# Kernel tuning notes

Measured on AMD Instinct MI355X. Metric: run time of the kernel, lower is better.

## Reference

```python
import jax, jax.numpy as jnp
import numpy as np

T = 2097152  # conversation length (even, per assert in the original forward)


def setup_inputs() -> dict:
    key = jax.random.key(0)
    k0, k1, k2, k3, k4, k5 = jax.random.split(key, 6)
    emission_scores = jax.random.normal(k0, (T, 2), dtype=jnp.float32)
    label = jax.random.randint(k1, (T,), 0, 2)
    who2who_state = jax.random.randint(k2, (T,), 0, 2)
    position_state = jax.random.randint(k3, (T,), 0, 19)
    # first step must use the zero (padding) transition matrix, per the original assert
    who2who_state = who2who_state.at[0].set(2)
    position_state = position_state.at[0].set(19)
    # learned params: matrice_u2s, matrice_s2u stacked; 19 position matrices stacked
    who2who_params = jax.random.normal(k4, (2, 2, 2), dtype=jnp.float32)
    position_params = jax.random.normal(k5, (19, 2, 2), dtype=jnp.float32)
    return dict(emission_scores=emission_scores, label=label,
                who2who_state=who2who_state, position_state=position_state,
                who2who_params=who2who_params, position_params=position_params)


def reference(emission_scores, label, who2who_state, position_state,
              who2who_params, position_params):
    dt = emission_scores.dtype
    pad = jnp.zeros((1, 2, 2), dtype=dt)
    who2who_sub = jnp.concatenate([who2who_params, pad], axis=0)    # [3,2,2]
    position_sub = jnp.concatenate([position_params, pad], axis=0)  # [20,2,2]
    # per-step combined transition matrices (Who2who_PositionCRF): [T,2,2]
    trans = who2who_sub[who2who_state] + position_sub[position_state]

    Tlen = emission_scores.shape[0]
    idx = jnp.arange(Tlen)
    sum_emission = jnp.sum(emission_scores[idx, label])
    # transitions are used for index > 0 with (label[t-1], label[t])
    sum_transition = jnp.sum(trans[1:][jnp.arange(Tlen - 1), label[:-1], label[1:]])
    gold_score = sum_emission + sum_transition

    # CRF forward (partition) recursion: alpha'[j] = logsumexp_i(alpha[i] + em[t,j] + trans[t,i,j])
    def step(alpha, xt):
        em_t, tr_t = xt  # [2], [2,2]
        new_alpha = jax.nn.logsumexp(alpha[:, None] + em_t[None, :] + tr_t, axis=0)
        return new_alpha, None

    alpha0 = jnp.zeros((2,), dtype=dt)
    alpha, _ = jax.lax.scan(step, alpha0, (emission_scores, trans))
    total_score = jax.nn.logsumexp(alpha)

    return jnp.stack([gold_score, total_score])
```

## Files before the change

kernel.cpp:

```cpp
#include <hip/hip_runtime.h>

#define T_LEN   2097152
#define CHUNK   8
#define BLOCK   256
#define NBLK    (T_LEN / (CHUNK * BLOCK))
#define NWAVE   (BLOCK / 64)
#define FINAL_PER (NBLK / 256)

#define LOG2E 1.44269504088896340736f
#define LN2   0.69314718055994530942f

__device__ __forceinline__ float fexp2(float x) {
#if __has_builtin(__builtin_amdgcn_exp2f)
    return __builtin_amdgcn_exp2f(x);
#else
    return __expf(x * LN2);
#endif
}
__device__ __forceinline__ float flog2(float x) {
#if __has_builtin(__builtin_amdgcn_logf)
    return __builtin_amdgcn_logf(x);
#else
    return __logf(x) * LOG2E;
#endif
}

__device__ __forceinline__ float lse2b(float x, float y) {
    float m = fmaxf(x, y);
    float d = fminf(x, y) - m;
    return m + flog2(1.0f + fexp2(d));
}

struct M2 { float a, b, c, d; };

__device__ __forceinline__ M2 mm(const M2 A, const M2 B) {
    M2 C;
    C.a = lse2b(A.a + B.a, A.b + B.c);
    C.b = lse2b(A.a + B.b, A.b + B.d);
    C.c = lse2b(A.c + B.a, A.d + B.c);
    C.d = lse2b(A.c + B.b, A.d + B.d);
    return C;
}

__device__ __forceinline__ void wave_reduce(M2& P, float& g, int lane) {
    #pragma unroll
    for (int m = 1; m < 64; m <<= 1) {
        M2 O;
        O.a = __shfl_xor(P.a, m);
        O.b = __shfl_xor(P.b, m);
        O.c = __shfl_xor(P.c, m);
        O.d = __shfl_xor(P.d, m);
        g  += __shfl_xor(g, m);
        bool hi = (lane & m) != 0;
        M2 X, Y;
        X.a = hi ? O.a : P.a;  X.b = hi ? O.b : P.b;
        X.c = hi ? O.c : P.c;  X.d = hi ? O.d : P.d;
        Y.a = hi ? P.a : O.a;  Y.b = hi ? P.b : O.b;
        Y.c = hi ? P.c : O.c;  Y.d = hi ? P.d : O.d;
        P = mm(X, Y);
    }
}

__global__ __launch_bounds__(BLOCK) void crf_partial(
    const float* __restrict__ em,
    const int*   __restrict__ label,
    const int*   __restrict__ wst,
    const int*   __restrict__ pst,
    const float* __restrict__ w2w,
    const float* __restrict__ pos,
    float* __restrict__ outP,
    float* __restrict__ outG)
{
    __shared__ float4 comb[60];
    __shared__ float4 wPs[NWAVE];
    __shared__ float  wGs[NWAVE];

    const int tid = threadIdx.x;
    if (tid < 60) {
        const int w = tid / 20, p = tid % 20;
        float v0 = 0.f, v1 = 0.f, v2 = 0.f, v3 = 0.f;
        if (w < 2)  { v0 += w2w[w*4+0]; v1 += w2w[w*4+1]; v2 += w2w[w*4+2]; v3 += w2w[w*4+3]; }
        if (p < 19) { v0 += pos[p*4+0]; v1 += pos[p*4+1]; v2 += pos[p*4+2]; v3 += pos[p*4+3]; }
        comb[tid] = make_float4(v0 * LOG2E, v1 * LOG2E, v2 * LOG2E, v3 * LOG2E);
    }
    __syncthreads();

    const int t0 = (blockIdx.x * BLOCK + tid) * CHUNK;

    const float4* emv = (const float4*)(em + 2 * (size_t)t0);
    float4 E0 = emv[0], E1 = emv[1], E2 = emv[2], E3 = emv[3];
    const int4* lv = (const int4*)(label + t0);
    const int4* wv = (const int4*)(wst   + t0);
    const int4* pv = (const int4*)(pst   + t0);
    int4 L0 = lv[0], L1 = lv[1];
    int4 W0 = wv[0], W1 = wv[1];
    int4 Pq0 = pv[0], Pq1 = pv[1];
    int prev = (t0 == 0) ? 0 : label[t0 - 1];

    E0.x *= LOG2E; E0.y *= LOG2E; E0.z *= LOG2E; E0.w *= LOG2E;
    E1.x *= LOG2E; E1.y *= LOG2E; E1.z *= LOG2E; E1.w *= LOG2E;
    E2.x *= LOG2E; E2.y *= LOG2E; E2.z *= LOG2E; E2.w *= LOG2E;
    E3.x *= LOG2E; E3.y *= LOG2E; E3.z *= LOG2E; E3.w *= LOG2E;

    float4 c0 = comb[W0.x*20 + Pq0.x];
    float4 c1 = comb[W0.y*20 + Pq0.y];
    float4 c2 = comb[W0.z*20 + Pq0.z];
    float4 c3 = comb[W0.w*20 + Pq0.w];
    float4 c4 = comb[W1.x*20 + Pq1.x];
    float4 c5 = comb[W1.y*20 + Pq1.y];
    float4 c6 = comb[W1.z*20 + Pq1.z];
    float4 c7 = comb[W1.w*20 + Pq1.w];

    float Pa, Pb, Pc, Pd, g;

    Pa = E0.x + c0.x;  Pb = E0.y + c0.y;
    Pc = E0.x + c0.z;  Pd = E0.y + c0.w;
    {
        const int l = L0.x;
        g  = l ? E0.y : E0.x;
        g += prev ? (l ? c0.w : c0.z) : (l ? c0.y : c0.x);
        prev = l;
    }

#define STEP(e0v, e1v, cc, ll)                                             \
    {                                                                      \
        const float e0 = (e0v), e1 = (e1v);                                \
        const float4 c = (cc);                                             \
        const int l = (ll);                                                \
        g += l ? e1 : e0;                                                  \
        g += prev ? (l ? c.w : c.z) : (l ? c.y : c.x);                     \
        prev = l;                                                          \
        float na = e0 + lse2b(Pa + c.x, Pb + c.z);                         \
        float nb = e1 + lse2b(Pa + c.y, Pb + c.w);                         \
        float nc = e0 + lse2b(Pc + c.x, Pd + c.z);                         \
        float nd = e1 + lse2b(Pc + c.y, Pd + c.w);                         \
        Pa = na; Pb = nb; Pc = nc; Pd = nd;                                \
    }

    STEP(E0.z, E0.w, c1, L0.y)
    STEP(E1.x, E1.y, c2, L0.z)
    STEP(E1.z, E1.w, c3, L0.w)
    STEP(E2.x, E2.y, c4, L1.x)
    STEP(E2.z, E2.w, c5, L1.y)
    STEP(E3.x, E3.y, c6, L1.z)
    STEP(E3.z, E3.w, c7, L1.w)
#undef STEP

    M2 P = { Pa, Pb, Pc, Pd };
    const int lane = tid & 63;
    wave_reduce(P, g, lane);

    const int wid = tid >> 6;
    if (lane == 0) { wPs[wid] = make_float4(P.a, P.b, P.c, P.d); wGs[wid] = g; }
    __syncthreads();
    if (tid == 0) {
        float4 q = wPs[0];
        M2 R = { q.x, q.y, q.z, q.w };
        float gg = wGs[0];
        #pragma unroll
        for (int w = 1; w < NWAVE; ++w) {
            float4 t = wPs[w];
            M2 B = { t.x, t.y, t.z, t.w };
            R = mm(R, B);
            gg += wGs[w];
        }
        ((float4*)outP)[blockIdx.x] = make_float4(R.a, R.b, R.c, R.d);
        outG[blockIdx.x] = gg;
    }
}

__global__ __launch_bounds__(256) void crf_final(
    const float* __restrict__ inP,
    const float* __restrict__ inG,
    float* __restrict__ out)
{
    __shared__ float4 wPs[4];
    __shared__ float  wGs[4];

    const int tid  = threadIdx.x;
    const int base = tid * FINAL_PER;

    float4 q = ((const float4*)inP)[base];
    M2 P = { q.x, q.y, q.z, q.w };
    float g = inG[base];
    #pragma unroll
    for (int k = 1; k < FINAL_PER; ++k) {
        float4 r = ((const float4*)inP)[base + k];
        M2 B = { r.x, r.y, r.z, r.w };
        P = mm(P, B);
        g += inG[base + k];
    }

    const int lane = tid & 63;
    wave_reduce(P, g, lane);

    const int wid = tid >> 6;
    if (lane == 0) { wPs[wid] = make_float4(P.a, P.b, P.c, P.d); wGs[wid] = g; }
    __syncthreads();
    if (tid == 0) {
        float4 q0 = wPs[0];
        M2 R = { q0.x, q0.y, q0.z, q0.w };
        float gg = wGs[0];
        #pragma unroll
        for (int w = 1; w < 4; ++w) {
            float4 t = wPs[w];
            M2 B = { t.x, t.y, t.z, t.w };
            R = mm(R, B);
            gg += wGs[w];
        }
        out[0] = gg * LN2;
        out[1] = lse2b(lse2b(R.a, R.b), lse2b(R.c, R.d)) * LN2;
    }
}

extern "C" void kernel_launch(void* const* d_in, const int* in_sizes, int n_in,
                              void* d_out, int out_size, void* d_ws, size_t ws_size,
                              hipStream_t stream) {
    const float* em    = (const float*)d_in[0];
    const int*   label = (const int*)  d_in[1];
    const int*   wst   = (const int*)  d_in[2];
    const int*   pst   = (const int*)  d_in[3];
    const float* w2w   = (const float*)d_in[4];
    const float* pos   = (const float*)d_in[5];
    float* out = (float*)d_out;

    float* outP = (float*)d_ws;
    float* outG = outP + NBLK * 4;

    crf_partial<<<NBLK, BLOCK, 0, stream>>>(em, label, wst, pst, w2w, pos, outP, outG);
    crf_final<<<1, 256, 0, stream>>>(outP, outG, out);
}
```

Measured before the change: 18.59 us.

## Switch CRF scan to linear-domain products with exponent renorm and fuse final reduction

The log-semiring 2x2 matrix products, which need an exp2/log2 pair per element, are replaced by ordinary linear-domain products. Emissions and transitions are exponentiated once, and overflow is managed by periodically pulling out power-of-two exponents into an integer. The chunk per thread is doubled to 16. The separate final kernel is replaced by a last-block-done atomic counter in the same kernel, which adds a memset launch. This cuts transcendental work and a kernel launch, at the cost of precision risk from linear-domain accumulation between renorms.

Result: slower. 29.94 us (+61.0%).

```diff
diff --git a/kernel.cpp b/kernel.cpp
--- a/kernel.cpp
+++ b/kernel.cpp
@@ -1,67 +1,60 @@
 #include <hip/hip_runtime.h>
 
 #define T_LEN   2097152
-#define CHUNK   8
+#define CHUNK   16
 #define BLOCK   256
 #define NBLK    (T_LEN / (CHUNK * BLOCK))
 #define NWAVE   (BLOCK / 64)
-#define FINAL_PER (NBLK / 256)
 
 #define LOG2E 1.44269504088896340736f
 #define LN2   0.69314718055994530942f
 
-__device__ __forceinline__ float fexp2(float x) {
 #if __has_builtin(__builtin_amdgcn_exp2f)
-    return __builtin_amdgcn_exp2f(x);
+__device__ __forceinline__ float fexp2(float x) { return __builtin_amdgcn_exp2f(x); }
 #else
-    return __expf(x * LN2);
+__device__ __forceinline__ float fexp2(float x) { return exp2f(x); }
 #endif
-}
-__device__ __forceinline__ float flog2(float x) {
 #if __has_builtin(__builtin_amdgcn_logf)
-    return __builtin_amdgcn_logf(x);
+__device__ __forceinline__ float flog2(float x) { return __builtin_amdgcn_logf(x); }
 #else
-    return __logf(x) * LOG2E;
+__device__ __forceinline__ float flog2(float x) { return log2f(x); }
 #endif
-}
-
-__device__ __forceinline__ float lse2b(float x, float y) {
-    float m = fmaxf(x, y);
-    float d = fminf(x, y) - m;
-    return m + flog2(1.0f + fexp2(d));
-}
-
-struct M2 { float a, b, c, d; };
-
-__device__ __forceinline__ M2 mm(const M2 A, const M2 B) {
-    M2 C;
-    C.a = lse2b(A.a + B.a, A.b + B.c);
-    C.b = lse2b(A.a + B.b, A.b + B.d);
-    C.c = lse2b(A.c + B.a, A.d + B.c);
-    C.d = lse2b(A.c + B.b, A.d + B.d);
-    return C;
-}
-
-__device__ __forceinline__ void wave_reduce(M2& P, float& g, int lane) {
+
+__device__ __forceinline__ void renorm4(float& a, float& b, float& c, float& d, int& e2) {
+    float mx = fmaxf(fmaxf(a, b), fmaxf(c, d));
+    int ex = (__float_as_int(mx) >> 23) & 0xff;
+    float s = __int_as_float((254 - ex) << 23);
+    a *= s; b *= s; c *= s; d *= s;
+    e2 += ex - 127;
+}
+__device__ __forceinline__ void renorm1(float& a, int& e2) {
+    int ex = (__float_as_int(a) >> 23) & 0xff;
+    float s = __int_as_float((254 - ex) << 23);
+    a *= s;
+    e2 += ex - 127;
+}
+
+__device__ __forceinline__ void wave_reduce_lin(float& Pa, float& Pb, float& Pc, float& Pd,
+                                                int& e2, float& g, int lane) {
     #pragma unroll
     for (int m = 1; m < 64; m <<= 1) {
-        M2 O;
-        O.a = __shfl_xor(P.a, m);
-        O.b = __shfl_xor(P.b, m);
-        O.c = __shfl_xor(P.c, m);
-        O.d = __shfl_xor(P.d, m);
-        g  += __shfl_xor(g, m);
-        bool hi = (lane & m) != 0;
-        M2 X, Y;
-        X.a = hi ? O.a : P.a;  X.b = hi ? O.b : P.b;
-        X.c = hi ? O.c : P.c;  X.d = hi ? O.d : P.d;
-        Y.a = hi ? P.a : O.a;  Y.b = hi ? P.b : O.b;
-        Y.c = hi ? P.c : O.c;  Y.d = hi ? P.d : O.d;
-        P = mm(X, Y);
-    }
-}
-
-__global__ __launch_bounds__(BLOCK) void crf_partial(
+        float Oa = __shfl_xor(Pa, m), Ob = __shfl_xor(Pb, m);
+        float Oc = __shfl_xor(Pc, m), Od = __shfl_xor(Pd, m);
+        int   Oe = __shfl_xor(e2, m);
+        g += __shfl_xor(g, m);
+        const bool hi = (lane & m) != 0;
+        float Xa = hi?Oa:Pa, Xb = hi?Ob:Pb, Xc = hi?Oc:Pc, Xd = hi?Od:Pd;
+        float Ya = hi?Pa:Oa, Yb = hi?Pb:Ob, Yc = hi?Pc:Oc, Yd = hi?Pd:Od;
+        Pa = Xa*Ya + Xb*Yc;
+        Pb = Xa*Yb + Xb*Yd;
+        Pc = Xc*Ya + Xd*Yc;
+        Pd = Xc*Yb + Xd*Yd;
+        e2 += Oe;
+        renorm4(Pa, Pb, Pc, Pd, e2);
+    }
+}
+
+__global__ __launch_bounds__(BLOCK) void crf_fused(
     const float* __restrict__ em,
     const int*   __restrict__ label,
     const int*   __restrict__ wst,
@@ -69,11 +62,16 @@
     const float* __restrict__ w2w,
     const float* __restrict__ pos,
     float* __restrict__ outP,
-    float* __restrict__ outG)
+    int*   __restrict__ outE,
+    float* __restrict__ outG,
+    unsigned* __restrict__ cnt,
+    float* __restrict__ out)
 {
-    __shared__ float4 comb[60];
+    __shared__ float4 combExp[60];
     __shared__ float4 wPs[NWAVE];
+    __shared__ int    wEs[NWAVE];
     __shared__ float  wGs[NWAVE];
+    __shared__ int    shLast;
 
     const int tid = threadIdx.x;
     if (tid < 60) {
@@ -81,7 +79,8 @@
         float v0 = 0.f, v1 = 0.f, v2 = 0.f, v3 = 0.f;
         if (w < 2)  { v0 += w2w[w*4+0]; v1 += w2w[w*4+1]; v2 += w2w[w*4+2]; v3 += w2w[w*4+3]; }
         if (p < 19) { v0 += pos[p*4+0]; v1 += pos[p*4+1]; v2 += pos[p*4+2]; v3 += pos[p*4+3]; }
-        comb[tid] = make_float4(v0 * LOG2E, v1 * LOG2E, v2 * LOG2E, v3 * LOG2E);
+        combExp[tid] = make_float4(fexp2(v0 * LOG2E), fexp2(v1 * LOG2E),
+                                   fexp2(v2 * LOG2E), fexp2(v3 * LOG2E));
     }
     __syncthreads();
 
@@ -89,128 +88,138 @@
 
     const float4* emv = (const float4*)(em + 2 * (size_t)t0);
     float4 E0 = emv[0], E1 = emv[1], E2 = emv[2], E3 = emv[3];
+    float4 E4 = emv[4], E5 = emv[5], E6 = emv[6], E7 = emv[7];
     const int4* lv = (const int4*)(label + t0);
     const int4* wv = (const int4*)(wst   + t0);
     const int4* pv = (const int4*)(pst   + t0);
-    int4 L0 = lv[0], L1 = lv[1];
-    int4 W0 = wv[0], W1 = wv[1];
-    int4 Pq0 = pv[0], Pq1 = pv[1];
+    int4 L0 = lv[0], L1 = lv[1], L2 = lv[2], L3 = lv[3];
+    int4 W0 = wv[0], W1 = wv[1], W2 = wv[2], W3 = wv[3];
+    int4 Q0 = pv[0], Q1 = pv[1], Q2 = pv[2], Q3 = pv[3];
     int prev = (t0 == 0) ? 0 : label[t0 - 1];
 
-    E0.x *= LOG2E; E0.y *= LOG2E; E0.z *= LOG2E; E0.w *= LOG2E;
-    E1.x *= LOG2E; E1.y *= LOG2E; E1.z *= LOG2E; E1.w *= LOG2E;
-    E2.x *= LOG2E; E2.y *= LOG2E; E2.z *= LOG2E; E2.w *= LOG2E;
-    E3.x *= LOG2E; E3.y *= LOG2E; E3.z *= LOG2E; E3.w *= LOG2E;
-
-    float4 c0 = comb[W0.x*20 + Pq0.x];
-    float4 c1 = comb[W0.y*20 + Pq0.y];
-    float4 c2 = comb[W0.z*20 + Pq0.z];
-    float4 c3 = comb[W0.w*20 + Pq0.w];
-    float4 c4 = comb[W1.x*20 + Pq1.x];
-    float4 c5 = comb[W1.y*20 + Pq1.y];
-    float4 c6 = comb[W1.z*20 + Pq1.z];
-    float4 c7 = comb[W1.w*20 + Pq1.w];
-
-    float Pa, Pb, Pc, Pd, g;
-
-    Pa = E0.x + c0.x;  Pb = E0.y + c0.y;
-    Pc = E0.x + c0.z;  Pd = E0.y + c0.w;
-    {
-        const int l = L0.x;
-        g  = l ? E0.y : E0.x;
-        g += prev ? (l ? c0.w : c0.z) : (l ? c0.y : c0.x);
-        prev = l;
-    }
-
-#define STEP(e0v, e1v, cc, ll)                                             \
+    float Pa = 1.f, Pb = 0.f, Pc = 0.f, Pd = 1.f;
+    int   e2 = 0;
+    float gEm  = 0.f;
+    float gLin = 1.f;
+    int   eg   = 0;
+
+#define STEP(e0v, e1v, wI, pI, lI)                                         \
     {                                                                      \
         const float e0 = (e0v), e1 = (e1v);                                \
-        const float4 c = (cc);                                             \
-        const int l = (ll);                                                \
-        g += l ? e1 : e0;                                                  \
-        g += prev ? (l ? c.w : c.z) : (l ? c.y : c.x);                     \
+        const float f0 = fexp2(e0 * LOG2E);                                \
+        const float f1 = fexp2(e1 * LOG2E);                                \
+        const float4 X = combExp[(wI)*20 + (pI)];                          \
+        const int l = (lI);                                                \
+        gEm += l ? e1 : e0;                                                \
+        gLin *= prev ? (l ? X.w : X.z) : (l ? X.y : X.x);                  \
         prev = l;                                                          \
-        float na = e0 + lse2b(Pa + c.x, Pb + c.z);                         \
-        float nb = e1 + lse2b(Pa + c.y, Pb + c.w);                         \
-        float nc = e0 + lse2b(Pc + c.x, Pd + c.z);                         \
-        float nd = e1 + lse2b(Pc + c.y, Pd + c.w);                         \
+        float na = (Pa*X.x + Pb*X.z) * f0;                                 \
+        float nb = (Pa*X.y + Pb*X.w) * f1;                                 \
+        float nc = (Pc*X.x + Pd*X.z) * f0;                                 \
+        float nd = (Pc*X.y + Pd*X.w) * f1;                                 \
         Pa = na; Pb = nb; Pc = nc; Pd = nd;                                \
     }
-
-    STEP(E0.z, E0.w, c1, L0.y)
-    STEP(E1.x, E1.y, c2, L0.z)
-    STEP(E1.z, E1.w, c3, L0.w)
-    STEP(E2.x, E2.y, c4, L1.x)
-    STEP(E2.z, E2.w, c5, L1.y)
-    STEP(E3.x, E3.y, c6, L1.z)
-    STEP(E3.z, E3.w, c7, L1.w)
+#define GROUP(Ea, Eb, L, W, Q)                                             \
+    STEP(Ea.x, Ea.y, W.x, Q.x, L.x)                                        \
+    STEP(Ea.z, Ea.w, W.y, Q.y, L.y)                                        \
+    STEP(Eb.x, Eb.y, W.z, Q.z, L.z)                                        \
+    STEP(Eb.z, Eb.w, W.w, Q.w, L.w)                                        \
+    renorm4(Pa, Pb, Pc, Pd, e2);                                           \
+    renorm1(gLin, eg);
+
+    GROUP(E0, E1, L0, W0, Q0)
+    GROUP(E2, E3, L1, W1, Q1)
+    GROUP(E4, E5, L2, W2, Q2)
+    GROUP(E6, E7, L3, W3, Q3)
+#undef GROUP
 #undef STEP
 
-    M2 P = { Pa, Pb, Pc, Pd };
+    float g = gEm + ((float)eg + flog2(gLin)) * LN2;
+
     const int lane = tid & 63;
-    wave_reduce(P, g, lane);
+    wave_reduce_lin(Pa, Pb, Pc, Pd, e2, g, lane);
 
     const int wid = tid >> 6;
-    if (lane == 0) { wPs[wid] = make_float4(P.a, P.b, P.c, P.d); wGs[wid] = g; }
+    if (lane == 0) { wPs[wid] = make_float4(Pa, Pb, Pc, Pd); wEs[wid] = e2; wGs[wid] = g; }
     __syncthreads();
     if (tid == 0) {
         float4 q = wPs[0];
-        M2 R = { q.x, q.y, q.z, q.w };
-        float gg = wGs[0];
+        float Ra = q.x, Rb = q.y, Rc = q.z, Rd = q.w;
+        int   re = wEs[0];
+        float rg = wGs[0];
         #pragma unroll
         for (int w = 1; w < NWAVE; ++w) {
             float4 t = wPs[w];
-            M2 B = { t.x, t.y, t.z, t.w };
-            R = mm(R, B);
-            gg += wGs[w];
+            float Ba = t.x, Bb = t.y, Bc = t.z, Bd = t.w;
+            float Ca = Ra*Ba + Rb*Bc;
+            float Cb = Ra*Bb + Rb*Bd;
+            float Cc = Rc*Ba + Rd*Bc;
+            float Cd = Rc*Bb + Rd*Bd;
+            Ra = Ca; Rb = Cb; Rc = Cc; Rd = Cd;
+            re += wEs[w];
+            renorm4(Ra, Rb, Rc, Rd, re);
+            rg += wGs[w];
         }
-        ((float4*)outP)[blockIdx.x] = make_float4(R.a, R.b, R.c, R.d);
-        outG[blockIdx.x] = gg;
-    }
-}
-
-__global__ __launch_bounds__(256) void crf_final(
-    const float* __restrict__ inP,
-    const float* __restrict__ inG,
-    float* __restrict__ out)
-{
-    __shared__ float4 wPs[4];
-    __shared__ float  wGs[4];
-
-    const int tid  = threadIdx.x;
-    const int base = tid * FINAL_PER;
-
-    float4 q = ((const float4*)inP)[base];
-    M2 P = { q.x, q.y, q.z, q.w };
-    float g = inG[base];
-    #pragma unroll
-    for (int k = 1; k < FINAL_PER; ++k) {
-        float4 r = ((const float4*)inP)[base + k];
-        M2 B = { r.x, r.y, r.z, r.w };
-        P = mm(P, B);
-        g += inG[base + k];
-    }
-
-    const int lane = tid & 63;
-    wave_reduce(P, g, lane);
-
-    const int wid = tid >> 6;
-    if (lane == 0) { wPs[wid] = make_float4(P.a, P.b, P.c, P.d); wGs[wid] = g; }
+        ((float4*)outP)[blockIdx.x] = make_float4(Ra, Rb, Rc, Rd);
+        outE[blockIdx.x] = re;
+        outG[blockIdx.x] = rg;
+    }
+
+    if (tid == 0) {
+        __threadfence();
+        unsigned old = atomicAdd(cnt, 1u);
+        shLast = (old == NBLK - 1) ? 1 : 0;
+    }
     __syncthreads();
-    if (tid == 0) {
-        float4 q0 = wPs[0];
-        M2 R = { q0.x, q0.y, q0.z, q0.w };
-        float gg = wGs[0];
-        #pragma unroll
-        for (int w = 1; w < 4; ++w) {
-            float4 t = wPs[w];
-            M2 B = { t.x, t.y, t.z, t.w };
-            R = mm(R, B);
-            gg += wGs[w];
+    if (!shLast) return;
+    __threadfence();
+
+#define ALDF(p) __hip_atomic_load((p), __ATOMIC_RELAXED, __HIP_MEMORY_SCOPE_AGENT)
+    {
+        const int i0 = 2 * tid, i1 = i0 + 1;
+        float Aa = ALDF(outP + 4*i0 + 0), Ab = ALDF(outP + 4*i0 + 1);
+        float Ac = ALDF(outP + 4*i0 + 2), Ad = ALDF(outP + 4*i0 + 3);
+        float Ba = ALDF(outP + 4*i1 + 0), Bb = ALDF(outP + 4*i1 + 1);
+        float Bc = ALDF(outP + 4*i1 + 2), Bd = ALDF(outP + 4*i1 + 3);
+        int   ea = ALDF(outE + i0), eb = ALDF(outE + i1);
+        float ga = ALDF(outG + i0), gb = ALDF(outG + i1);
+
+        float Pa2 = Aa*Ba + Ab*Bc;
+        float Pb2 = Aa*Bb + Ab*Bd;
+        float Pc2 = Ac*Ba + Ad*Bc;
+        float Pd2 = Ac*Bb + Ad*Bd;
+        int   e2f = ea + eb;
+        renorm4(Pa2, Pb2, Pc2, Pd2, e2f);
+        float gf = ga + gb;
+
+        wave_reduce_lin(Pa2, Pb2, Pc2, Pd2, e2f, gf, lane);
+
+        __syncthreads();
+        if (lane == 0) { wPs[wid] = make_float4(Pa2, Pb2, Pc2, Pd2); wEs[wid] = e2f; wGs[wid] = gf; }
+        __syncthreads();
+        if (tid == 0) {
+            float4 q = wPs[0];
+            float Ra = q.x, Rb = q.y, Rc = q.z, Rd = q.w;
+            int   re = wEs[0];
+            float rg = wGs[0];
+            #pragma unroll
+            for (int w = 1; w < NWAVE; ++w) {
+                float4 t = wPs[w];
+                float Ba2 = t.x, Bb2 = t.y, Bc2 = t.z, Bd2 = t.w;
+                float Ca = Ra*Ba2 + Rb*Bc2;
+                float Cb = Ra*Bb2 + Rb*Bd2;
+                float Cc = Rc*Ba2 + Rd*Bc2;
+                float Cd = Rc*Bb2 + Rd*Bd2;
+                Ra = Ca; Rb = Cb; Rc = Cc; Rd = Cd;
+                re += wEs[w];
+                renorm4(Ra, Rb, Rc, Rd, re);
+                rg += wGs[w];
+            }
+            out[0] = rg;
+            out[1] = ((float)re + flog2(Ra + Rb + Rc + Rd)) * LN2;
         }
-        out[0] = gg * LN2;
-        out[1] = lse2b(lse2b(R.a, R.b), lse2b(R.c, R.d)) * LN2;
-    }
+    }
+#undef ALDF
 }
 
 extern "C" void kernel_launch(void* const* d_in, const int* in_sizes, int n_in,
@@ -224,9 +233,13 @@
     const float* pos   = (const float*)d_in[5];
     float* out = (float*)d_out;
 
-    float* outP = (float*)d_ws;
-    float* outG = outP + NBLK * 4;
-
-    crf_partial<<<NBLK, BLOCK, 0, stream>>>(em, label, wst, pst, w2w, pos, outP, outG);
-    crf_final<<<1, 256, 0, stream>>>(outP, outG, out);
-}
+    float*    outP = (float*)d_ws;
+    int*      outE = (int*)(outP + NBLK * 4);
+    float*    outG = (float*)(outE + NBLK);
+    unsigned* cnt  = (unsigned*)(outG + NBLK);
+
+    hipMemsetAsync(cnt, 0, sizeof(unsigned), stream);
+
+    crf_fused<<<NBLK, BLOCK, 0, stream>>>(em, label, wst, pst, w2w, pos,
+                                          outP, outE, outG, cnt, out);
+}
```
